# Performance work log

Measured on AMD Instinct MI355X. Metric: run time of the kernel, lower is better.

## Reference

```python
import jax, jax.numpy as jnp
import numpy as np

H = 12      # heads
P = 4       # dim_point
CHUNK = 256 # chunk_size
DIM_SINGLE = 768
DIM_PAIR = 64
B, N = 1, 1024


def setup_inputs() -> dict:
    key = jax.random.key(0)
    ks = jax.random.split(key, 24)
    s = 0.02
    d = DIM_SINGLE
    inp = {
        'single': jax.random.normal(ks[0], (B, N, d), jnp.float32),
        'pair': jax.random.normal(ks[1], (B, N, N, DIM_PAIR), jnp.float32),
        'rot': jax.random.normal(ks[2], (B, N, 3, 3), jnp.float32),
        'trans': jax.random.normal(ks[3], (B, N, 3), jnp.float32),
        # Linear weights stored as (in, out) so y = x @ W + b
        'Wq': jax.random.normal(ks[4], (d, d), jnp.float32) * s,
        'bq': jnp.zeros((d,), jnp.float32),
        'Wk': jax.random.normal(ks[5], (d, d), jnp.float32) * s,
        'bk': jnp.zeros((d,), jnp.float32),
        'Wv': jax.random.normal(ks[6], (d, d), jnp.float32) * s,
        'bv': jnp.zeros((d,), jnp.float32),
        'Wpb': jax.random.normal(ks[7], (DIM_PAIR, H), jnp.float32) * s,
        'bpb': jnp.zeros((H,), jnp.float32),
        'Wqp': jax.random.normal(ks[8], (d, H * P * 3), jnp.float32) * s,
        'bqp': jnp.zeros((H * P * 3,), jnp.float32),
        'Wkp': jax.random.normal(ks[9], (d, H * P * 3), jnp.float32) * s,
        'bkp': jnp.zeros((H * P * 3,), jnp.float32),
        'Wvp': jax.random.normal(ks[10], (d, H * P * 3), jnp.float32) * s,
        'bvp': jnp.zeros((H * P * 3,), jnp.float32),
        'Wo': jax.random.normal(ks[11], (d, d), jnp.float32) * s,
        'bo': jnp.zeros((d,), jnp.float32),
        'Wpo': jax.random.normal(ks[12], (H * P * 3, d), jnp.float32) * s,
        'bpo': jnp.zeros((d,), jnp.float32),
        'ln_g': jnp.ones((d,), jnp.float32),
        'ln_b': jnp.zeros((d,), jnp.float32),
    }
    return inp


def _layernorm(x, g, b, eps=1e-5):
    mu = jnp.mean(x, axis=-1, keepdims=True)
    var = jnp.mean((x - mu) ** 2, axis=-1, keepdims=True)
    return (x - mu) * jax.lax.rsqrt(var + eps) * g + b


def reference(single, pair, rot, trans, Wq, bq, Wk, bk, Wv, bv, Wpb, bpb,
              Wqp, bqp, Wkp, bkp, Wvp, bvp, Wo, bo, Wpo, bpo, ln_g, ln_b):
    Bs, Ns, C = single.shape
    Ch = C // H
    scale = Ch ** (-0.5)

    q = (single @ Wq + bq).reshape(Bs, Ns, H, Ch)
    k = (single @ Wk + bk).reshape(Bs, Ns, H, Ch)
    v = (single @ Wv + bv).reshape(Bs, Ns, H, Ch)

    # [B,N,N,H] -> [B,H,N,M]
    pair_bias = jnp.transpose(pair @ Wpb + bpb, (0, 3, 1, 2))

    q_pts = (single @ Wqp + bqp).reshape(Bs, Ns, H, P, 3)
    k_pts = (single @ Wkp + bkp).reshape(Bs, Ns, H, P, 3)
    v_pts = (single @ Wvp + bvp).reshape(Bs, Ns, H, P, 3)

    t = trans[:, :, None, None, :]  # [B,N,1,1,3]
    q_pts_g = jnp.einsum('bnhpd,bnde->bnhpe', q_pts, rot) + t
    k_pts_g = jnp.einsum('bnhpd,bnde->bnhpe', k_pts, rot) + t
    v_pts_g = jnp.einsum('bnhpd,bnde->bnhpe', v_pts, rot) + t

    q2_h = jnp.transpose(jnp.sum(q_pts_g ** 2, axis=(3, 4)), (0, 2, 1))  # [B,H,N]
    k2_h = jnp.transpose(jnp.sum(k_pts_g ** 2, axis=(3, 4)), (0, 2, 1))  # [B,H,N]

    scalar_logits = jnp.einsum('bnhc,bmhc->bhnm', q, k) * scale  # [B,H,N,N]

    out_scalar = jnp.zeros((Bs, Ns, H, Ch), single.dtype)
    out_points = jnp.zeros((Bs, Ns, H, P, 3), single.dtype)

    # Faithful to the original: softmax is taken PER CHUNK over the key axis,
    # and the per-chunk weighted sums are accumulated.
    for start in range(0, Ns, CHUNK):
        end = min(start + CHUNK, Ns)
        qk = jnp.einsum('bnhpd,bmhpd->bhnm', q_pts_g, k_pts_g[:, start:end])
        pt_logits = -0.5 * (q2_h[:, :, :, None] + k2_h[:, :, None, start:end]
                            - 2.0 * qk) * scale
        logits = scalar_logits[:, :, :, start:end] + pair_bias[:, :, :, start:end] + pt_logits
        attn = jax.nn.softmax(logits, axis=-1)  # [B,H,N,chunk]
        out_scalar = out_scalar + jnp.einsum('bhnm,bmhc->bnhc', attn, v[:, start:end])
        out_points = out_points + jnp.einsum('bhnm,bmhpd->bnhpd', attn, v_pts_g[:, start:end])

    weighted_scalar = out_scalar.reshape(Bs, Ns, H * Ch)
    weighted_points = out_points.reshape(Bs, Ns, H * P * 3)
    point_proj = weighted_points @ Wpo + bpo
    out = (weighted_scalar + point_proj) @ Wo + bo
    return _layernorm(single + out, ln_g, ln_b)
```

## Files before the change

kernel.cpp:

```cpp
#include <hip/hip_runtime.h>
#include <stdint.h>

#define NTOK 1024
#define NH 12

typedef short bf16x8 __attribute__((ext_vector_type(8)));
typedef float f32x4 __attribute__((ext_vector_type(4)));
typedef uint32_t u32x4 __attribute__((ext_vector_type(4)));

__device__ __forceinline__ unsigned short f2bf(float f) {
  union { float f; uint32_t u; } x; x.f = f;
  uint32_t r = x.u + 0x7FFFu + ((x.u >> 16) & 1u);
  return (unsigned short)(r >> 16);
}
__device__ __forceinline__ float bf2f(unsigned short u) {
  union { uint32_t u; float f; } x; x.u = ((uint32_t)u) << 16;
  return x.f;
}
__device__ __forceinline__ bf16x8 pack8(float4 a, float4 b) {
  bf16x8 r;
  r[0] = (short)f2bf(a.x); r[1] = (short)f2bf(a.y);
  r[2] = (short)f2bf(a.z); r[3] = (short)f2bf(a.w);
  r[4] = (short)f2bf(b.x); r[5] = (short)f2bf(b.y);
  r[6] = (short)f2bf(b.z); r[7] = (short)f2bf(b.w);
  return r;
}

__global__ __launch_bounds__(256) void prep_k(
    const float* __restrict__ single, const float* __restrict__ Wq,
    const float* __restrict__ Wk, const float* __restrict__ Wv,
    const float* __restrict__ Wqp, const float* __restrict__ Wkp,
    const float* __restrict__ Wvp, const float* __restrict__ Wpo,
    const float* __restrict__ Wo, const float* __restrict__ Wpb,
    const float* __restrict__ bq, const float* __restrict__ bk,
    const float* __restrict__ bv, const float* __restrict__ bqp,
    const float* __restrict__ bkp, const float* __restrict__ bvp,
    unsigned short* __restrict__ sgl, unsigned short* __restrict__ wcat,
    unsigned short* __restrict__ wpo, unsigned short* __restrict__ wo,
    float* __restrict__ bcat, unsigned short* __restrict__ wpbt)
{
  int idx = blockIdx.x * 256 + threadIdx.x;
  const int S0 = 786432;
  const int SW = 589824;
  const int SP = 110592;
  if (idx < S0) { sgl[idx] = f2bf(single[idx]); return; }
  idx -= S0;
  if (idx < 3 * SW) {
    int j = idx / SW, o = idx % SW;
    int n = o / 768, k = o % 768;
    const float* W = (j == 0) ? Wq : (j == 1) ? Wk : Wv;
    wcat[((size_t)(j * 768 + n)) * 768 + k] = f2bf(W[k * 768 + n]);
    return;
  }
  idx -= 3 * SW;
  if (idx < 3 * SP) {
    int j = idx / SP, o = idx % SP;
    int n = o / 768, k = o % 768;
    const float* W = (j == 0) ? Wqp : (j == 1) ? Wkp : Wvp;
    wcat[((size_t)(2304 + j * 144 + n)) * 768 + k] = f2bf(W[k * 144 + n]);
    return;
  }
  idx -= 3 * SP;
  if (idx < SP) {
    int n = idx / 144, k = idx % 144;
    wpo[idx] = f2bf(Wpo[k * 768 + n]);
    return;
  }
  idx -= SP;
  if (idx < SW) {
    int n = idx / 768, k = idx % 768;
    wo[idx] = f2bf(Wo[k * 768 + n]);
    return;
  }
  idx -= SW;
  if (idx < 2736) {
    float v;
    if (idx < 768) v = bq[idx];
    else if (idx < 1536) v = bk[idx - 768];
    else if (idx < 2304) v = bv[idx - 1536];
    else if (idx < 2448) v = bqp[idx - 2304];
    else if (idx < 2592) v = bkp[idx - 2448];
    else v = bvp[idx - 2592];
    bcat[idx] = v;
    return;
  }
  idx -= 2736;
  if (idx < 1024) {
    int h = idx >> 6, k = idx & 63;
    wpbt[idx] = (h < 12) ? f2bf(Wpb[k * 12 + h]) : (unsigned short)0;
    return;
  }
}

template <int MODE>
__global__ __launch_bounds__(256) void gemm_bt_k(
    const unsigned short* __restrict__ A, int lda,
    const unsigned short* __restrict__ Bt, int ldb,
    int Nact, int kmax, int ktiles,
    float* __restrict__ outf, unsigned short* __restrict__ outb, int ldc,
    const float* __restrict__ p0, const float* __restrict__ p1)
{
  __shared__ unsigned short As[128 * 32];
  __shared__ unsigned short Bs[128 * 32];
  const int t = threadIdx.x;
  const int w = t >> 6, lane = t & 63;
  const int wr = w >> 1, wc = w & 1;
  const int lr = lane & 15, lc = lane >> 4;
  const int m0 = blockIdx.x * 128, n0 = blockIdx.y * 128;

  const int s0 = t, s1 = t + 256;
  const int r0 = s0 >> 2, c0 = s0 & 3, r1 = s1 >> 2, c1 = s1 & 3;

  f32x4 acc[4][4] = {};
  u32x4 zz = {0u, 0u, 0u, 0u};
  u32x4 pa0, pa1, pq0, pq1;

#define LOAD_AB(KT)                                                              \
  do {                                                                           \
    int k0_ = (KT) * 32;                                                         \
    int g0_ = k0_ + c0 * 8, g1_ = k0_ + c1 * 8;                                  \
    pa0 = (g0_ < kmax) ? *(const u32x4*)(A + (size_t)(m0 + r0) * lda + g0_) : zz; \
    pa1 = (g1_ < kmax) ? *(const u32x4*)(A + (size_t)(m0 + r1) * lda + g1_) : zz; \
    pq0 = (g0_ < kmax && (n0 + r0) < Nact)                                       \
              ? *(const u32x4*)(Bt + (size_t)(n0 + r0) * ldb + g0_) : zz;        \
    pq1 = (g1_ < kmax && (n0 + r1) < Nact)                                       \
              ? *(const u32x4*)(Bt + (size_t)(n0 + r1) * ldb + g1_) : zz;        \
  } while (0)

  LOAD_AB(0);
  for (int kt = 0; kt < ktiles; ++kt) {
    __syncthreads();
    ((u32x4*)As)[r0 * 4 + c0] = pa0;
    ((u32x4*)As)[r1 * 4 + c1] = pa1;
    ((u32x4*)Bs)[r0 * 4 + c0] = pq0;
    ((u32x4*)Bs)[r1 * 4 + c1] = pq1;
    __syncthreads();
    if (kt + 1 < ktiles) LOAD_AB(kt + 1);

    bf16x8 af[4], bfr[4];
#pragma unroll
    for (int mi = 0; mi < 4; ++mi) {
      int row = wr * 64 + mi * 16 + lr;
      af[mi] = *(const bf16x8*)(As + (row * 4 + lc) * 8);
    }
#pragma unroll
    for (int ni = 0; ni < 4; ++ni) {
      int row = wc * 64 + ni * 16 + lr;
      bfr[ni] = *(const bf16x8*)(Bs + (row * 4 + lc) * 8);
    }
#pragma unroll
    for (int mi = 0; mi < 4; ++mi)
#pragma unroll
      for (int ni = 0; ni < 4; ++ni)
        acc[mi][ni] = __builtin_amdgcn_mfma_f32_16x16x32_bf16(
            af[mi], bfr[ni], acc[mi][ni], 0, 0, 0);
  }
#undef LOAD_AB

#pragma unroll
  for (int mi = 0; mi < 4; ++mi) {
#pragma unroll
    for (int ni = 0; ni < 4; ++ni) {
#pragma unroll
      for (int r = 0; r < 4; ++r) {
        int row = m0 + wr * 64 + mi * 16 + lc * 4 + r;
        int col = n0 + wc * 64 + ni * 16 + lr;
        if (col < Nact) {
          float v = acc[mi][ni][r];
          if constexpr (MODE == 0) {
            outf[(size_t)row * ldc + col] = v + p0[col];
          } else {
            float sv = v + p0[col] + p1[(size_t)row * 768 + col];
            outb[(size_t)row * ldc + col] = f2bf(sv);
          }
        }
      }
    }
  }
}

__global__ __launch_bounds__(256) void rotate_k(
    const float* __restrict__ qp, const float* __restrict__ rot,
    const float* __restrict__ trans,
    unsigned short* __restrict__ Acat, unsigned short* __restrict__ Bcat,
    unsigned short* __restrict__ VcatT, float* __restrict__ q2k2)
{
  const int n = blockIdx.x, t = threadIdx.x;
  __shared__ float R[9], T[3], rg[432];
  if (t < 9) R[t] = rot[n * 9 + t];
  if (t >= 9 && t < 12) T[t - 9] = trans[n * 3 + (t - 9)];
  __syncthreads();
  for (int s = t; s < 432; s += 256) {
    int j = s / 144, r = s % 144;
    int h = r / 12, wo = r % 12;
    int e = wo % 3;
    size_t base = (size_t)n * 2736 + 2304 + j * 144 + (r - e);
    float d0 = qp[base + 0], d1 = qp[base + 1], d2 = qp[base + 2];
    float val = d0 * R[e] + d1 * R[3 + e] + d2 * R[6 + e] + T[e];
    rg[s] = val;
    unsigned short bv = f2bf(val);
    if (j == 0)      Acat[((size_t)h * NTOK + n) * 96 + 64 + wo] = bv;
    else if (j == 1) Bcat[((size_t)h * NTOK + n) * 96 + 64 + wo] = bv;
    else             VcatT[((size_t)h * 80 + 64 + wo) * NTOK + n] = bv;
  }
  __syncthreads();
  for (int s = t; s < 2304; s += 256) {
    int j = s / 768, c = s % 768;
    int h = c >> 6, cc = c & 63;
    unsigned short bv = f2bf(qp[(size_t)n * 2736 + s]);
    if (j == 0)      Acat[((size_t)h * NTOK + n) * 96 + cc] = bv;
    else if (j == 1) Bcat[((size_t)h * NTOK + n) * 96 + cc] = bv;
    else             VcatT[((size_t)h * 80 + cc) * NTOK + n] = bv;
  }
  if (t < 240) {
    int h = t / 20, ix = 76 + t % 20;
    Acat[((size_t)h * NTOK + n) * 96 + ix] = 0;
    Bcat[((size_t)h * NTOK + n) * 96 + ix] = 0;
  }
  if (t >= 240 && t < 288) {
    int s = t - 240;
    int h = s / 4, rr = 76 + s % 4;
    VcatT[((size_t)h * 80 + rr) * NTOK + n] = 0;
  }
  if (t < 24) {
    int j = t / 12, h = t % 12;
    float sum = 0.f;
#pragma unroll
    for (int wo = 0; wo < 12; ++wo) {
      float v = rg[j * 144 + h * 12 + wo];
      sum += v * v;
    }
    q2k2[(size_t)(j * NH + h) * NTOK + n] = sum;
  }
}

__global__ __launch_bounds__(256) void pairbias_k(
    const float* __restrict__ pair, const unsigned short* __restrict__ wpbt,
    const float* __restrict__ bpb, const float* __restrict__ q2k2,
    unsigned short* __restrict__ pb)
{
  const int t = threadIdx.x, w = t >> 6, lane = t & 63;
  const int lr = lane & 15, g = lane >> 4;
  bf16x8 wf0 = *(const bf16x8*)(wpbt + lr * 64 + g * 8);
  bf16x8 wf1 = *(const bf16x8*)(wpbt + lr * 64 + 32 + g * 8);
  const float bias_h = (lr < 12) ? bpb[lr] : 0.f;
  const int wid = blockIdx.x * 4 + w;
#pragma unroll
  for (int it = 0; it < 4; ++it) {
    int tile = wid * 4 + it;
    int nm0 = tile * 16;
    int n = nm0 >> 10;
    int m0_ = nm0 & 1023;
    const float* src = pair + (size_t)(nm0 + lr) * 64 + g * 8;
    float4 aA = *(const float4*)(src);
    float4 aB = *(const float4*)(src + 4);
    float4 aC = *(const float4*)(src + 32);
    float4 aD = *(const float4*)(src + 36);
    bf16x8 f0 = pack8(aA, aB);
    bf16x8 f1 = pack8(aC, aD);
    f32x4 c = {0.f, 0.f, 0.f, 0.f};
    c = __builtin_amdgcn_mfma_f32_16x16x32_bf16(f0, wf0, c, 0, 0, 0);
    c = __builtin_amdgcn_mfma_f32_16x16x32_bf16(f1, wf1, c, 0, 0, 0);
    if (lr < 12) {
      float q2v = q2k2[lr * 1024 + n];
      float4 k2v = *(const float4*)(q2k2 + (12 + lr) * 1024 + m0_ + g * 4);
      ushort4 o;
      o.x = f2bf(c[0] + bias_h - 0.0625f * (q2v + k2v.x));
      o.y = f2bf(c[1] + bias_h - 0.0625f * (q2v + k2v.y));
      o.z = f2bf(c[2] + bias_h - 0.0625f * (q2v + k2v.z));
      o.w = f2bf(c[3] + bias_h - 0.0625f * (q2v + k2v.w));
      *(ushort4*)(pb + ((size_t)lr << 20) + (size_t)nm0 + g * 4) = o;
    }
  }
}

__global__ __launch_bounds__(256) void attn_k(
    const unsigned short* __restrict__ pb, const unsigned short* __restrict__ Acat,
    const unsigned short* __restrict__ Bcat, const unsigned short* __restrict__ VcatT,
    float* __restrict__ acc4)
{
  __shared__ unsigned short Ls[64 * 256];
  __shared__ unsigned short Bs[128 * 104];
  const int t = threadIdx.x, w = t >> 6, lane = t & 63;
  const int lr = lane & 15, lc = lane >> 4;
  const int n0 = blockIdx.x * 64;
  const int m0 = blockIdx.y * 256;
  const int h  = blockIdx.z;

  const unsigned short* Pg = pb + ((size_t)h << 20) + (size_t)n0 * 1024 + m0;
#pragma unroll
  for (int i = 0; i < 8; ++i) {
    int idx = i * 256 + t;
    int row = idx >> 5, sl = idx & 31;
    u32x4 v = *(const u32x4*)(Pg + (size_t)row * 1024 + sl * 8);
    ((u32x4*)Ls)[row * 32 + (sl ^ (row & 7))] = v;
  }
  const unsigned short* Kg = Bcat + ((size_t)h * 1024 + m0) * 96;
#pragma unroll
  for (int i = 0; i < 6; ++i) {
    int idx = i * 256 + t;
    int row = idx / 12, c = idx % 12;
    u32x4 v = *(const u32x4*)(Kg + (size_t)row * 96 + c * 8);
    *(u32x4*)(Bs + row * 104 + c * 8) = v;
  }
  __syncthreads();

  bf16x8 qf[3];
  const unsigned short* Qg = Acat + ((size_t)h * 1024 + n0 + w * 16 + lr) * 96;
#pragma unroll
  for (int kk = 0; kk < 3; ++kk) qf[kk] = *(const bf16x8*)(Qg + kk * 32 + lc * 8);

  f32x4 sa[16];
#pragma unroll
  for (int ct = 0; ct < 16; ++ct) sa[ct] = (f32x4){0.f, 0.f, 0.f, 0.f};

#pragma unroll
  for (int ct = 0; ct < 8; ++ct)
#pragma unroll
    for (int kk = 0; kk < 3; ++kk) {
      bf16x8 kf = *(const bf16x8*)(Bs + (ct * 16 + lr) * 104 + kk * 32 + lc * 8);
      sa[ct] = __builtin_amdgcn_mfma_f32_16x16x32_bf16(kf, qf[kk], sa[ct], 0, 0, 0);
    }
  __syncthreads();
#pragma unroll
  for (int i = 0; i < 6; ++i) {
    int idx = i * 256 + t;
    int row = idx / 12, c = idx % 12;
    u32x4 v = *(const u32x4*)(Kg + (size_t)(128 + row) * 96 + c * 8);
    *(u32x4*)(Bs + row * 104 + c * 8) = v;
  }
  __syncthreads();
#pragma unroll
  for (int ct = 8; ct < 16; ++ct)
#pragma unroll
    for (int kk = 0; kk < 3; ++kk) {
      bf16x8 kf = *(const bf16x8*)(Bs + ((ct - 8) * 16 + lr) * 104 + kk * 32 + lc * 8);
      sa[ct] = __builtin_amdgcn_mfma_f32_16x16x32_bf16(kf, qf[kk], sa[ct], 0, 0, 0);
    }

  const int nrow = w * 16 + lr;
  float lg[16][4];
  float mx = -1e30f;
#pragma unroll
  for (int ct = 0; ct < 16; ++ct) {
    int sl = (ct * 2 + (lc >> 1)) ^ (nrow & 7);
    const unsigned short* p = Ls + nrow * 256 + sl * 8 + (lc & 1) * 4;
    ushort4 pv = *(const ushort4*)p;
    lg[ct][0] = 0.125f * sa[ct][0] + bf2f(pv.x);
    lg[ct][1] = 0.125f * sa[ct][1] + bf2f(pv.y);
    lg[ct][2] = 0.125f * sa[ct][2] + bf2f(pv.z);
    lg[ct][3] = 0.125f * sa[ct][3] + bf2f(pv.w);
    mx = fmaxf(mx, fmaxf(fmaxf(lg[ct][0], lg[ct][1]), fmaxf(lg[ct][2], lg[ct][3])));
  }
  mx = fmaxf(mx, __shfl_xor(mx, 16, 64));
  mx = fmaxf(mx, __shfl_xor(mx, 32, 64));
  float sm = 0.f;
#pragma unroll
  for (int ct = 0; ct < 16; ++ct)
#pragma unroll
    for (int r = 0; r < 4; ++r) { lg[ct][r] = __expf(lg[ct][r] - mx); sm += lg[ct][r]; }
  sm += __shfl_xor(sm, 16, 64);
  sm += __shfl_xor(sm, 32, 64);
  float inv = 1.0f / sm;
#pragma unroll
  for (int ct = 0; ct < 16; ++ct) {
    int sl = (ct * 2 + (lc >> 1)) ^ (nrow & 7);
    unsigned short* p = Ls + nrow * 256 + sl * 8 + (lc & 1) * 4;
    ushort4 pw;
    pw.x = f2bf(lg[ct][0] * inv); pw.y = f2bf(lg[ct][1] * inv);
    pw.z = f2bf(lg[ct][2] * inv); pw.w = f2bf(lg[ct][3] * inv);
    *(ushort4*)p = pw;
  }
  __syncthreads();

  f32x4 acc[5];
#pragma unroll
  for (int nf = 0; nf < 5; ++nf) acc[nf] = (f32x4){0.f, 0.f, 0.f, 0.f};
  const unsigned short* Vg = VcatT + (size_t)h * 80 * NTOK + m0;
#pragma unroll
  for (int kk = 0; kk < 8; ++kk) {
    int row = w * 16 + lr;
    int sl = (kk * 4 + lc) ^ (row & 7);
    bf16x8 a = *(const bf16x8*)(Ls + row * 256 + sl * 8);
#pragma unroll
    for (int nf = 0; nf < 5; ++nf) {
      int c = nf * 16 + lr;
      bf16x8 b = *(const bf16x8*)(Vg + (size_t)c * NTOK + kk * 32 + lc * 8);
      acc[nf] = __builtin_amdgcn_mfma_f32_16x16x32_bf16(a, b, acc[nf], 0, 0, 0);
    }
  }
  float* out = acc4 + ((size_t)blockIdx.y * NH + h) * (size_t)NTOK * 80;
#pragma unroll
  for (int nf = 0; nf < 5; ++nf)
#pragma unroll
    for (int r = 0; r < 4; ++r) {
      int orow = n0 + w * 16 + lc * 4 + r;
      int c = nf * 16 + lr;
      out[(size_t)orow * 80 + c] = acc[nf][r];
    }
}

__global__ __launch_bounds__(256) void reduce_out_k(
    const float* __restrict__ acc4, unsigned short* __restrict__ wp,
    float* __restrict__ wsum)
{
  int idx = blockIdx.x * 256 + threadIdx.x;
  if (idx >= 1024 * 912) return;
  int n = idx / 912, c = idx % 912;
  const size_t cs = (size_t)NH * NTOK * 80;
  if (c < 768) {
    int h = c >> 6, cc = c & 63;
    size_t base = ((size_t)h * NTOK + n) * 80 + cc;
    float v = acc4[base] + acc4[base + cs] + acc4[base + 2 * cs] + acc4[base + 3 * cs];
    wsum[(size_t)n * 768 + c] = v;
  } else {
    int c2 = c - 768;
    int h = c2 / 12, wo = c2 % 12;
    size_t base = ((size_t)h * NTOK + n) * 80 + 64 + wo;
    float v = acc4[base] + acc4[base + cs] + acc4[base + 2 * cs] + acc4[base + 3 * cs];
    wp[(size_t)n * 144 + c2] = f2bf(v);
  }
}

__global__ __launch_bounds__(256) void ln_k(
    const float* __restrict__ single, const float* __restrict__ outpre,
    const float* __restrict__ g, const float* __restrict__ b,
    float* __restrict__ out)
{
  const int row = blockIdx.x, t = threadIdx.x;
  __shared__ float red[8];
  size_t base = (size_t)row * 768;
  float x0 = single[base + t] + outpre[base + t];
  float x1 = single[base + t + 256] + outpre[base + t + 256];
  float x2 = single[base + t + 512] + outpre[base + t + 512];
  float s = x0 + x1 + x2;
#pragma unroll
  for (int off = 32; off; off >>= 1) s += __shfl_xor(s, off, 64);
  if ((t & 63) == 0) red[t >> 6] = s;
  __syncthreads();
  float mu = (red[0] + red[1] + red[2] + red[3]) * (1.0f / 768.0f);
  float d0 = x0 - mu, d1 = x1 - mu, d2 = x2 - mu;
  float vs = d0 * d0 + d1 * d1 + d2 * d2;
#pragma unroll
  for (int off = 32; off; off >>= 1) vs += __shfl_xor(vs, off, 64);
  if ((t & 63) == 0) red[4 + (t >> 6)] = vs;
  __syncthreads();
  float var = (red[4] + red[5] + red[6] + red[7]) * (1.0f / 768.0f);
  float rs = rsqrtf(var + 1e-5f);
  out[base + t]       = d0 * rs * g[t]       + b[t];
  out[base + t + 256] = d1 * rs * g[t + 256] + b[t + 256];
  out[base + t + 512] = d2 * rs * g[t + 512] + b[t + 512];
}

extern "C" void kernel_launch(void* const* d_in, const int* in_sizes, int n_in,
                              void* d_out, int out_size, void* d_ws, size_t ws_size,
                              hipStream_t stream)
{
  (void)in_sizes; (void)n_in; (void)out_size; (void)ws_size;
  const float* single = (const float*)d_in[0];
  const float* pair   = (const float*)d_in[1];
  const float* rot    = (const float*)d_in[2];
  const float* trans  = (const float*)d_in[3];
  const float* Wq  = (const float*)d_in[4];  const float* bq  = (const float*)d_in[5];
  const float* Wk  = (const float*)d_in[6];  const float* bk  = (const float*)d_in[7];
  const float* Wv  = (const float*)d_in[8];  const float* bv  = (const float*)d_in[9];
  const float* Wpb = (const float*)d_in[10]; const float* bpb = (const float*)d_in[11];
  const float* Wqp = (const float*)d_in[12]; const float* bqp = (const float*)d_in[13];
  const float* Wkp = (const float*)d_in[14]; const float* bkp = (const float*)d_in[15];
  const float* Wvp = (const float*)d_in[16]; const float* bvp = (const float*)d_in[17];
  const float* Wo  = (const float*)d_in[18]; const float* bo  = (const float*)d_in[19];
  const float* Wpo = (const float*)d_in[20]; const float* bpo = (const float*)d_in[21];
  const float* lng = (const float*)d_in[22]; const float* lnb = (const float*)d_in[23];

  char* ws = (char*)d_ws;
  unsigned short* sgl    = (unsigned short*)(ws + 0);
  unsigned short* wcat   = (unsigned short*)(ws + 1572864);
  unsigned short* wpo_   = (unsigned short*)(ws + 5775360);
  unsigned short* wo_    = (unsigned short*)(ws + 5996544);
  float*          bcat   = (float*)(ws + 7176192);
  unsigned short* wpbt   = (unsigned short*)(ws + 7187136);
  float*          qp     = (float*)(ws + 7189504);
  unsigned short* Acat   = (unsigned short*)(ws + 18396160);
  unsigned short* Bcat   = (unsigned short*)(ws + 20755456);
  unsigned short* VcatT  = (unsigned short*)(ws + 23114752);
  float*          q2k2   = (float*)(ws + 25080832);
  unsigned short* pb     = (unsigned short*)(ws + 25179136);
  float*          acc4   = (float*)(ws + 50344960);
  unsigned short* wp     = (unsigned short*)(ws + 66073600);
  float*          wsum   = (float*)(ws + 66368512);
  unsigned short* S      = (unsigned short*)(ws + 69514240);
  float*          outpre = (float*)(ws + 71087104);

  prep_k<<<14031, 256, 0, stream>>>(single, Wq, Wk, Wv, Wqp, Wkp, Wvp, Wpo, Wo,
                                    Wpb, bq, bk, bv, bqp, bkp, bvp,
                                    sgl, wcat, wpo_, wo_, bcat, wpbt);

  gemm_bt_k<0><<<dim3(8, 22, 1), 256, 0, stream>>>(
      sgl, 768, wcat, 768, 2736, 768, 24, qp, nullptr, 2736, bcat, nullptr);

  rotate_k<<<1024, 256, 0, stream>>>(qp, rot, trans, Acat, Bcat, VcatT, q2k2);

  pairbias_k<<<4096, 256, 0, stream>>>(pair, wpbt, bpb, q2k2, pb);

  attn_k<<<dim3(16, 4, 12), 256, 0, stream>>>(pb, Acat, Bcat, VcatT, acc4);

  reduce_out_k<<<3648, 256, 0, stream>>>(acc4, wp, wsum);

  gemm_bt_k<3><<<dim3(8, 6, 1), 256, 0, stream>>>(
      wp, 144, wpo_, 144, 768, 144, 5, nullptr, S, 768, bpo, wsum);

  gemm_bt_k<0><<<dim3(8, 6, 1), 256, 0, stream>>>(
      S, 768, wo_, 768, 768, 768, 24, outpre, nullptr, 768, bo, nullptr);

  ln_k<<<1024, 256, 0, stream>>>(single, outpre, lng, lnb, (float*)d_out);
}
```

Measured before the change: 196.0 us.

## Fold point projection into output weight and merge QKV GEMM with pair-bias kernel

Precomputes the fused weight Wpo·Wo (plus fused bias) so the tail becomes a single split-K GEMM over a concatenated 912-wide activation instead of two chained GEMMs. The QKV projection GEMM is split-K in two slabs and launched in one heterogeneous kernel together with the pair-bias projection and the weight fusion, removing launches and idle tails. The q²/k² point terms move from the pair-bias kernel into the attention kernel. The cost is extra partial-sum reads in rotate and layernorm, plus an extra bf16 rounding of the fused weight.

```diff
diff --git a/kernel.cpp b/kernel.cpp
--- a/kernel.cpp
+++ b/kernel.cpp
@@ -3,6 +3,7 @@
 
 #define NTOK 1024
 #define NH 12
+#define QPSLAB 2801664
 
 typedef short bf16x8 __attribute__((ext_vector_type(8)));
 typedef float f32x4 __attribute__((ext_vector_type(4)));
@@ -36,7 +37,7 @@
     const float* __restrict__ bv, const float* __restrict__ bqp,
     const float* __restrict__ bkp, const float* __restrict__ bvp,
     unsigned short* __restrict__ sgl, unsigned short* __restrict__ wcat,
-    unsigned short* __restrict__ wpo, unsigned short* __restrict__ wo,
+    unsigned short* __restrict__ WB, unsigned short* __restrict__ wpoA,
     float* __restrict__ bcat, unsigned short* __restrict__ wpbt)
 {
   int idx = blockIdx.x * 256 + threadIdx.x;
@@ -61,18 +62,17 @@
     return;
   }
   idx -= 3 * SP;
-  if (idx < SP) {
-    int n = idx / 144, k = idx % 144;
-    wpo[idx] = f2bf(Wpo[k * 768 + n]);
-    return;
-  }
-  idx -= SP;
   if (idx < SW) {
     int n = idx / 768, k = idx % 768;
-    wo[idx] = f2bf(Wo[k * 768 + n]);
+    WB[(size_t)n * 912 + k] = f2bf(Wo[k * 768 + n]);
     return;
   }
   idx -= SW;
+  if (idx < SP) {
+    wpoA[idx] = f2bf(Wpo[idx]);
+    return;
+  }
+  idx -= SP;
   if (idx < 2736) {
     float v;
     if (idx < 768) v = bq[idx];
@@ -92,24 +92,22 @@
   }
 }
 
-template <int MODE>
-__global__ __launch_bounds__(256) void gemm_bt_k(
-    const unsigned short* __restrict__ A, int lda,
-    const unsigned short* __restrict__ Bt, int ldb,
-    int Nact, int kmax, int ktiles,
+template <int EPI>
+__device__ __forceinline__ void gemm_dev(
+    unsigned short* As, unsigned short* Bs,
+    const unsigned short* __restrict__ A, int lda, int Mact,
+    const unsigned short* __restrict__ Bt, int ldb, int Nact,
+    int kt0, int ktn, int kmax,
     float* __restrict__ outf, unsigned short* __restrict__ outb, int ldc,
-    const float* __restrict__ p0, const float* __restrict__ p1)
-{
-  __shared__ unsigned short As[128 * 32];
-  __shared__ unsigned short Bs[128 * 32];
+    const float* __restrict__ p0, int mb, int nb, int addbias)
+{
   const int t = threadIdx.x;
   const int w = t >> 6, lane = t & 63;
   const int wr = w >> 1, wc = w & 1;
   const int lr = lane & 15, lc = lane >> 4;
-  const int m0 = blockIdx.x * 128, n0 = blockIdx.y * 128;
-
-  const int s0 = t, s1 = t + 256;
-  const int r0 = s0 >> 2, c0 = s0 & 3, r1 = s1 >> 2, c1 = s1 & 3;
+  const int m0 = mb * 128, n0 = nb * 128;
+  const int r0 = t >> 2, c0 = t & 3;
+  const int r1 = r0 + 64;
 
   f32x4 acc[4][4] = {};
   u32x4 zz = {0u, 0u, 0u, 0u};
@@ -118,24 +116,26 @@
 #define LOAD_AB(KT)                                                              \
   do {                                                                           \
     int k0_ = (KT) * 32;                                                         \
-    int g0_ = k0_ + c0 * 8, g1_ = k0_ + c1 * 8;                                  \
-    pa0 = (g0_ < kmax) ? *(const u32x4*)(A + (size_t)(m0 + r0) * lda + g0_) : zz; \
-    pa1 = (g1_ < kmax) ? *(const u32x4*)(A + (size_t)(m0 + r1) * lda + g1_) : zz; \
+    int g0_ = k0_ + c0 * 8;                                                      \
+    pa0 = (g0_ < kmax && (m0 + r0) < Mact)                                       \
+              ? *(const u32x4*)(A + (size_t)(m0 + r0) * lda + g0_) : zz;         \
+    pa1 = (g0_ < kmax && (m0 + r1) < Mact)                                       \
+              ? *(const u32x4*)(A + (size_t)(m0 + r1) * lda + g0_) : zz;         \
     pq0 = (g0_ < kmax && (n0 + r0) < Nact)                                       \
               ? *(const u32x4*)(Bt + (size_t)(n0 + r0) * ldb + g0_) : zz;        \
-    pq1 = (g1_ < kmax && (n0 + r1) < Nact)                                       \
-              ? *(const u32x4*)(Bt + (size_t)(n0 + r1) * ldb + g1_) : zz;        \
+    pq1 = (g0_ < kmax && (n0 + r1) < Nact)                                       \
+              ? *(const u32x4*)(Bt + (size_t)(n0 + r1) * ldb + g0_) : zz;        \
   } while (0)
 
-  LOAD_AB(0);
-  for (int kt = 0; kt < ktiles; ++kt) {
+  LOAD_AB(kt0);
+  for (int kt = kt0; kt < kt0 + ktn; ++kt) {
     __syncthreads();
     ((u32x4*)As)[r0 * 4 + c0] = pa0;
-    ((u32x4*)As)[r1 * 4 + c1] = pa1;
+    ((u32x4*)As)[r1 * 4 + c0] = pa1;
     ((u32x4*)Bs)[r0 * 4 + c0] = pq0;
-    ((u32x4*)Bs)[r1 * 4 + c1] = pq1;
+    ((u32x4*)Bs)[r1 * 4 + c0] = pq1;
     __syncthreads();
-    if (kt + 1 < ktiles) LOAD_AB(kt + 1);
+    if (kt + 1 < kt0 + ktn) LOAD_AB(kt + 1);
 
     bf16x8 af[4], bfr[4];
 #pragma unroll
@@ -165,13 +165,12 @@
       for (int r = 0; r < 4; ++r) {
         int row = m0 + wr * 64 + mi * 16 + lc * 4 + r;
         int col = n0 + wc * 64 + ni * 16 + lr;
-        if (col < Nact) {
+        if (row < Mact && col < Nact) {
           float v = acc[mi][ni][r];
-          if constexpr (MODE == 0) {
-            outf[(size_t)row * ldc + col] = v + p0[col];
+          if constexpr (EPI == 0) {
+            outf[(size_t)row * ldc + col] = addbias ? (v + p0[col]) : v;
           } else {
-            float sv = v + p0[col] + p1[(size_t)row * 768 + col];
-            outb[(size_t)row * ldc + col] = f2bf(sv);
+            outb[(size_t)col * 912 + 768 + row] = f2bf(v);
           }
         }
       }
@@ -179,8 +178,77 @@
   }
 }
 
+__global__ __launch_bounds__(256) void fat_k(
+    const unsigned short* __restrict__ sgl, const unsigned short* __restrict__ wcat,
+    const float* __restrict__ bcat, float* __restrict__ qp2,
+    const float* __restrict__ pair, const unsigned short* __restrict__ wpbt,
+    const float* __restrict__ bpb, unsigned short* __restrict__ pb,
+    const unsigned short* __restrict__ wpoA, unsigned short* __restrict__ WB,
+    const float* __restrict__ bpo, const float* __restrict__ Wo,
+    const float* __restrict__ bo, float* __restrict__ bfused)
+{
+  __shared__ unsigned short As[128 * 32];
+  __shared__ unsigned short Bs[128 * 32];
+  const int bid = blockIdx.x;
+  const int t = threadIdx.x;
+
+  if (bid < 12) {
+    int mb = bid & 1, nb = bid >> 1;
+    gemm_dev<1>(As, Bs, wpoA, 768, 144, WB, 912, 768, 0, 24, 768,
+                nullptr, WB, 912, nullptr, mb, nb, 0);
+    return;
+  }
+  if (bid < 15) {
+    int n = (bid - 12) * 256 + t;
+    float s = bo[n];
+    for (int j = 0; j < 768; ++j) s += bpo[j] * Wo[(size_t)j * 768 + n];
+    bfused[n] = s;
+    return;
+  }
+  if (bid < 367) {
+    int pbid = bid - 15;
+    int zk = pbid / 176, rem = pbid % 176;
+    int mb = rem & 7, nb = rem >> 3;
+    gemm_dev<0>(As, Bs, sgl, 768, 1024, wcat, 768, 2736,
+                zk * 12, 12, 768,
+                qp2 + (size_t)zk * QPSLAB, nullptr, 2736, bcat, mb, nb, zk == 0);
+    return;
+  }
+  {
+    const int w = t >> 6, lane = t & 63;
+    const int lr = lane & 15, g = lane >> 4;
+    bf16x8 wf0 = *(const bf16x8*)(wpbt + lr * 64 + g * 8);
+    bf16x8 wf1 = *(const bf16x8*)(wpbt + lr * 64 + 32 + g * 8);
+    const float bias_h = (lr < 12) ? bpb[lr] : 0.f;
+    const int wid = (bid - 367) * 4 + w;
+#pragma unroll
+    for (int it = 0; it < 4; ++it) {
+      int tile = wid * 4 + it;
+      int nm0 = tile * 16;
+      const float* src = pair + (size_t)(nm0 + lr) * 64 + g * 8;
+      float4 aA = *(const float4*)(src);
+      float4 aB = *(const float4*)(src + 4);
+      float4 aC = *(const float4*)(src + 32);
+      float4 aD = *(const float4*)(src + 36);
+      bf16x8 f0 = pack8(aA, aB);
+      bf16x8 f1 = pack8(aC, aD);
+      f32x4 c = {0.f, 0.f, 0.f, 0.f};
+      c = __builtin_amdgcn_mfma_f32_16x16x32_bf16(f0, wf0, c, 0, 0, 0);
+      c = __builtin_amdgcn_mfma_f32_16x16x32_bf16(f1, wf1, c, 0, 0, 0);
+      if (lr < 12) {
+        ushort4 o;
+        o.x = f2bf(c[0] + bias_h);
+        o.y = f2bf(c[1] + bias_h);
+        o.z = f2bf(c[2] + bias_h);
+        o.w = f2bf(c[3] + bias_h);
+        *(ushort4*)(pb + ((size_t)lr << 20) + (size_t)nm0 + g * 4) = o;
+      }
+    }
+  }
+}
+
 __global__ __launch_bounds__(256) void rotate_k(
-    const float* __restrict__ qp, const float* __restrict__ rot,
+    const float* __restrict__ qp2, const float* __restrict__ rot,
     const float* __restrict__ trans,
     unsigned short* __restrict__ Acat, unsigned short* __restrict__ Bcat,
     unsigned short* __restrict__ VcatT, float* __restrict__ q2k2)
@@ -195,7 +263,9 @@
     int h = r / 12, wo = r % 12;
     int e = wo % 3;
     size_t base = (size_t)n * 2736 + 2304 + j * 144 + (r - e);
-    float d0 = qp[base + 0], d1 = qp[base + 1], d2 = qp[base + 2];
+    float d0 = qp2[base + 0] + qp2[base + 0 + QPSLAB];
+    float d1 = qp2[base + 1] + qp2[base + 1 + QPSLAB];
+    float d2 = qp2[base + 2] + qp2[base + 2 + QPSLAB];
     float val = d0 * R[e] + d1 * R[3 + e] + d2 * R[6 + e] + T[e];
     rg[s] = val;
     unsigned short bv = f2bf(val);
@@ -207,7 +277,8 @@
   for (int s = t; s < 2304; s += 256) {
     int j = s / 768, c = s % 768;
     int h = c >> 6, cc = c & 63;
-    unsigned short bv = f2bf(qp[(size_t)n * 2736 + s]);
+    size_t ix = (size_t)n * 2736 + s;
+    unsigned short bv = f2bf(qp2[ix] + qp2[ix + QPSLAB]);
     if (j == 0)      Acat[((size_t)h * NTOK + n) * 96 + cc] = bv;
     else if (j == 1) Bcat[((size_t)h * NTOK + n) * 96 + cc] = bv;
     else             VcatT[((size_t)h * 80 + cc) * NTOK + n] = bv;
@@ -234,50 +305,10 @@
   }
 }
 
-__global__ __launch_bounds__(256) void pairbias_k(
-    const float* __restrict__ pair, const unsigned short* __restrict__ wpbt,
-    const float* __restrict__ bpb, const float* __restrict__ q2k2,
-    unsigned short* __restrict__ pb)
-{
-  const int t = threadIdx.x, w = t >> 6, lane = t & 63;
-  const int lr = lane & 15, g = lane >> 4;
-  bf16x8 wf0 = *(const bf16x8*)(wpbt + lr * 64 + g * 8);
-  bf16x8 wf1 = *(const bf16x8*)(wpbt + lr * 64 + 32 + g * 8);
-  const float bias_h = (lr < 12) ? bpb[lr] : 0.f;
-  const int wid = blockIdx.x * 4 + w;
-#pragma unroll
-  for (int it = 0; it < 4; ++it) {
-    int tile = wid * 4 + it;
-    int nm0 = tile * 16;
-    int n = nm0 >> 10;
-    int m0_ = nm0 & 1023;
-    const float* src = pair + (size_t)(nm0 + lr) * 64 + g * 8;
-    float4 aA = *(const float4*)(src);
-    float4 aB = *(const float4*)(src + 4);
-    float4 aC = *(const float4*)(src + 32);
-    float4 aD = *(const float4*)(src + 36);
-    bf16x8 f0 = pack8(aA, aB);
-    bf16x8 f1 = pack8(aC, aD);
-    f32x4 c = {0.f, 0.f, 0.f, 0.f};
-    c = __builtin_amdgcn_mfma_f32_16x16x32_bf16(f0, wf0, c, 0, 0, 0);
-    c = __builtin_amdgcn_mfma_f32_16x16x32_bf16(f1, wf1, c, 0, 0, 0);
-    if (lr < 12) {
-      float q2v = q2k2[lr * 1024 + n];
-      float4 k2v = *(const float4*)(q2k2 + (12 + lr) * 1024 + m0_ + g * 4);
-      ushort4 o;
-      o.x = f2bf(c[0] + bias_h - 0.0625f * (q2v + k2v.x));
-      o.y = f2bf(c[1] + bias_h - 0.0625f * (q2v + k2v.y));
-      o.z = f2bf(c[2] + bias_h - 0.0625f * (q2v + k2v.z));
-      o.w = f2bf(c[3] + bias_h - 0.0625f * (q2v + k2v.w));
-      *(ushort4*)(pb + ((size_t)lr << 20) + (size_t)nm0 + g * 4) = o;
-    }
-  }
-}
-
 __global__ __launch_bounds__(256) void attn_k(
     const unsigned short* __restrict__ pb, const unsigned short* __restrict__ Acat,
     const unsigned short* __restrict__ Bcat, const unsigned short* __restrict__ VcatT,
-    float* __restrict__ acc4)
+    const float* __restrict__ q2k2, float* __restrict__ acc4)
 {
   __shared__ unsigned short Ls[64 * 256];
   __shared__ unsigned short Bs[128 * 104];
@@ -339,6 +370,8 @@
     }
 
   const int nrow = w * 16 + lr;
+  const float q2v = q2k2[(size_t)h * 1024 + n0 + nrow];
+  const float* k2b = q2k2 + 12288 + (size_t)h * 1024 + m0;
   float lg[16][4];
   float mx = -1e30f;
 #pragma unroll
@@ -346,10 +379,11 @@
     int sl = (ct * 2 + (lc >> 1)) ^ (nrow & 7);
     const unsigned short* p = Ls + nrow * 256 + sl * 8 + (lc & 1) * 4;
     ushort4 pv = *(const ushort4*)p;
-    lg[ct][0] = 0.125f * sa[ct][0] + bf2f(pv.x);
-    lg[ct][1] = 0.125f * sa[ct][1] + bf2f(pv.y);
-    lg[ct][2] = 0.125f * sa[ct][2] + bf2f(pv.z);
-    lg[ct][3] = 0.125f * sa[ct][3] + bf2f(pv.w);
+    float4 k2v = *(const float4*)(k2b + ct * 16 + lc * 4);
+    lg[ct][0] = 0.125f * sa[ct][0] + bf2f(pv.x) - 0.0625f * (q2v + k2v.x);
+    lg[ct][1] = 0.125f * sa[ct][1] + bf2f(pv.y) - 0.0625f * (q2v + k2v.y);
+    lg[ct][2] = 0.125f * sa[ct][2] + bf2f(pv.z) - 0.0625f * (q2v + k2v.z);
+    lg[ct][3] = 0.125f * sa[ct][3] + bf2f(pv.w) - 0.0625f * (q2v + k2v.w);
     mx = fmaxf(mx, fmaxf(fmaxf(lg[ct][0], lg[ct][1]), fmaxf(lg[ct][2], lg[ct][3])));
   }
   mx = fmaxf(mx, __shfl_xor(mx, 16, 64));
@@ -400,39 +434,56 @@
     }
 }
 
-__global__ __launch_bounds__(256) void reduce_out_k(
-    const float* __restrict__ acc4, unsigned short* __restrict__ wp,
-    float* __restrict__ wsum)
+__global__ __launch_bounds__(256) void reduce_k(
+    const float* __restrict__ acc4, unsigned short* __restrict__ AW)
 {
   int idx = blockIdx.x * 256 + threadIdx.x;
-  if (idx >= 1024 * 912) return;
   int n = idx / 912, c = idx % 912;
   const size_t cs = (size_t)NH * NTOK * 80;
+  size_t base;
   if (c < 768) {
     int h = c >> 6, cc = c & 63;
-    size_t base = ((size_t)h * NTOK + n) * 80 + cc;
-    float v = acc4[base] + acc4[base + cs] + acc4[base + 2 * cs] + acc4[base + 3 * cs];
-    wsum[(size_t)n * 768 + c] = v;
+    base = ((size_t)h * NTOK + n) * 80 + cc;
   } else {
     int c2 = c - 768;
     int h = c2 / 12, wo = c2 % 12;
-    size_t base = ((size_t)h * NTOK + n) * 80 + 64 + wo;
-    float v = acc4[base] + acc4[base + cs] + acc4[base + 2 * cs] + acc4[base + 3 * cs];
-    wp[(size_t)n * 144 + c2] = f2bf(v);
-  }
+    base = ((size_t)h * NTOK + n) * 80 + 64 + wo;
+  }
+  float v = acc4[base] + acc4[base + cs] + acc4[base + 2 * cs] + acc4[base + 3 * cs];
+  AW[(size_t)n * 912 + c] = f2bf(v);
+}
+
+__global__ __launch_bounds__(256) void tail_gemm_k(
+    const unsigned short* __restrict__ AW, const unsigned short* __restrict__ WB,
+    float* __restrict__ outpre)
+{
+  __shared__ unsigned short As[128 * 32];
+  __shared__ unsigned short Bs[128 * 32];
+  int z = blockIdx.z;
+  int kt0 = z * 8, ktn = (z < 3) ? 8 : 5;
+  gemm_dev<0>(As, Bs, AW, 912, 1024, WB, 912, 768, kt0, ktn, 912,
+              outpre + (size_t)z * 786432, nullptr, 768, nullptr,
+              blockIdx.x, blockIdx.y, 0);
 }
 
 __global__ __launch_bounds__(256) void ln_k(
     const float* __restrict__ single, const float* __restrict__ outpre,
-    const float* __restrict__ g, const float* __restrict__ b,
-    float* __restrict__ out)
+    const float* __restrict__ bfused, const float* __restrict__ g,
+    const float* __restrict__ b, float* __restrict__ out)
 {
   const int row = blockIdx.x, t = threadIdx.x;
   __shared__ float red[8];
   size_t base = (size_t)row * 768;
-  float x0 = single[base + t] + outpre[base + t];
-  float x1 = single[base + t + 256] + outpre[base + t + 256];
-  float x2 = single[base + t + 512] + outpre[base + t + 512];
+  const size_t SL = 786432;
+  float x0 = single[base + t] + bfused[t]
+           + outpre[base + t] + outpre[base + t + SL]
+           + outpre[base + t + 2 * SL] + outpre[base + t + 3 * SL];
+  float x1 = single[base + t + 256] + bfused[t + 256]
+           + outpre[base + t + 256] + outpre[base + t + 256 + SL]
+           + outpre[base + t + 256 + 2 * SL] + outpre[base + t + 256 + 3 * SL];
+  float x2 = single[base + t + 512] + bfused[t + 512]
+           + outpre[base + t + 512] + outpre[base + t + 512 + SL]
+           + outpre[base + t + 512 + 2 * SL] + outpre[base + t + 512 + 3 * SL];
   float s = x0 + x1 + x2;
 #pragma unroll
   for (int off = 32; off; off >>= 1) s += __shfl_xor(s, off, 64);
@@ -475,42 +526,35 @@
   char* ws = (char*)d_ws;
   unsigned short* sgl    = (unsigned short*)(ws + 0);
   unsigned short* wcat   = (unsigned short*)(ws + 1572864);
-  unsigned short* wpo_   = (unsigned short*)(ws + 5775360);
-  unsigned short* wo_    = (unsigned short*)(ws + 5996544);
-  float*          bcat   = (float*)(ws + 7176192);
-  unsigned short* wpbt   = (unsigned short*)(ws + 7187136);
-  float*          qp     = (float*)(ws + 7189504);
-  unsigned short* Acat   = (unsigned short*)(ws + 18396160);
-  unsigned short* Bcat   = (unsigned short*)(ws + 20755456);
-  unsigned short* VcatT  = (unsigned short*)(ws + 23114752);
-  float*          q2k2   = (float*)(ws + 25080832);
-  unsigned short* pb     = (unsigned short*)(ws + 25179136);
-  float*          acc4   = (float*)(ws + 50344960);
-  unsigned short* wp     = (unsigned short*)(ws + 66073600);
-  float*          wsum   = (float*)(ws + 66368512);
-  unsigned short* S      = (unsigned short*)(ws + 69514240);
-  float*          outpre = (float*)(ws + 71087104);
+  unsigned short* wpoA   = (unsigned short*)(ws + 5775360);
+  unsigned short* WB     = (unsigned short*)(ws + 5996544);
+  float*          bcat   = (float*)(ws + 7397376);
+  unsigned short* wpbt   = (unsigned short*)(ws + 7408384);
+  float*          bfused = (float*)(ws + 7410432);
+  float*          qp2    = (float*)(ws + 7413504);
+  unsigned short* Acat   = (unsigned short*)(ws + 29826816);
+  unsigned short* Bcat   = (unsigned short*)(ws + 32186112);
+  unsigned short* VcatT  = (unsigned short*)(ws + 34545408);
+  float*          q2k2   = (float*)(ws + 36511488);
+  unsigned short* pb     = (unsigned short*)(ws + 36609792);
+  float*          acc4   = (float*)(ws + 61775616);
+  unsigned short* AW     = (unsigned short*)(ws + 77504256);
+  float*          outpre = (float*)(ws + 79372032);
 
   prep_k<<<14031, 256, 0, stream>>>(single, Wq, Wk, Wv, Wqp, Wkp, Wvp, Wpo, Wo,
                                     Wpb, bq, bk, bv, bqp, bkp, bvp,
-                                    sgl, wcat, wpo_, wo_, bcat, wpbt);
-
-  gemm_bt_k<0><<<dim3(8, 22, 1), 256, 0, stream>>>(
-      sgl, 768, wcat, 768, 2736, 768, 24, qp, nullptr, 2736, bcat, nullptr);
-
-  rotate_k<<<1024, 256, 0, stream>>>(qp, rot, trans, Acat, Bcat, VcatT, q2k2);
-
-  pairbias_k<<<4096, 256, 0, stream>>>(pair, wpbt, bpb, q2k2, pb);
-
-  attn_k<<<dim3(16, 4, 12), 256, 0, stream>>>(pb, Acat, Bcat, VcatT, acc4);
-
-  reduce_out_k<<<3648, 256, 0, stream>>>(acc4, wp, wsum);
-
-  gemm_bt_k<3><<<dim3(8, 6, 1), 256, 0, stream>>>(
-      wp, 144, wpo_, 144, 768, 144, 5, nullptr, S, 768, bpo, wsum);
-
-  gemm_bt_k<0><<<dim3(8, 6, 1), 256, 0, stream>>>(
-      S, 768, wo_, 768, 768, 768, 24, outpre, nullptr, 768, bo, nullptr);
-
-  ln_k<<<1024, 256, 0, stream>>>(single, outpre, lng, lnb, (float*)d_out);
-}
+                                    sgl, wcat, WB, wpoA, bcat, wpbt);
+
+  fat_k<<<4463, 256, 0, stream>>>(sgl, wcat, bcat, qp2, pair, wpbt, bpb, pb,
+                                  wpoA, WB, bpo, Wo, bo, bfused);
+
+  rotate_k<<<1024, 256, 0, stream>>>(qp2, rot, trans, Acat, Bcat, VcatT, q2k2);
+
+  attn_k<<<dim3(16, 4, 12), 256, 0, stream>>>(pb, Acat, Bcat, VcatT, q2k2, acc4);
+
+  reduce_k<<<3648, 256, 0, stream>>>(acc4, AW);
+
+  tail_gemm_k<<<dim3(8, 6, 4), 256, 0, stream>>>(AW, WB, outpre);
+
+  ln_k<<<1024, 256, 0, stream>>>(single, outpre, bfused, lng, lnb, (float*)d_out);
+}
```

Measured after the change: 169.2 us. 1.16x faster.
